# Performance work log

Hardware: AMD Instinct MI355X
Metric: run time of the kernel (lower is better)

## Reference

```python
import jax, jax.numpy as jnp
import numpy as np

SIGMA = 0.248
PRNUM = 6
P = 7.5
K = 3.0
ALPHA = 2.5


def _gauss_kernel():
    # 5x5 normalized Gaussian, replicated per channel for depthwise conv [O=3,I=1,5,5]
    x = jnp.arange(-2, 3, dtype=jnp.float32)
    x2, y2 = jnp.meshgrid(x, x, indexing='xy')
    k = jnp.exp(-(x2 ** 2 + y2 ** 2) / (2.0 * SIGMA ** 2))
    k = k / jnp.sum(k)
    return jnp.broadcast_to(k[None, None], (3, 1, 5, 5))


def _dwconv(x, k):
    # x: [3,H,W]; depthwise 5x5 conv, padding=2 (matches F.conv2d(..., padding=2, groups=3))
    return jax.lax.conv_general_dilated(
        x[None], k, window_strides=(1, 1), padding=[(2, 2), (2, 2)],
        feature_group_count=3, dimension_numbers=('NCHW', 'OIHW', 'NCHW'))[0]


def _down2(x):
    # torch bilinear align_corners=False at exact scale 0.5 == 2x2 average pooling
    c, h, w = x.shape
    return x.reshape(c, h // 2, 2, w // 2, 2).mean(axis=(2, 4))


def _up(x, hw):
    # torch bilinear align_corners=False upsample (half-pixel centers) == jax linear resize
    return jax.image.resize(x, (x.shape[0], hw[0], hw[1]), method='linear')


def _foveate(img, fixs):
    C, H, W = img.shape
    k = _gauss_kernel()
    # build Gaussian pyramid
    G = img
    pyr = [G]
    for _ in range(1, PRNUM):
        G = _down2(_dwconv(G, k))
        pyr.append(G)
    # re-expand each level back to full res (interpolate then blur at each step)
    As = [pyr[0]]
    for i in range(1, PRNUM):
        cur = pyr[i]
        for j in range(i):
            hw = (cur.shape[1] * 2, cur.shape[2] * 2) if j < i - 1 else (H, W)
            cur = _dwconv(_up(cur, hw), k)
        As.append(cur)
    As = jnp.stack(As)  # [prNum, 3, H, W]

    # radial eccentricity map (min distance over fixations)
    x = jnp.arange(W, dtype=jnp.float32)
    y = jnp.arange(H, dtype=jnp.float32)
    x2d, y2d = jnp.meshgrid(x, y, indexing='xy')  # each [H, W]
    d = jnp.sqrt((x2d[None] - fixs[:, 0, None, None]) ** 2 +
                 (y2d[None] - fixs[:, 1, None, None]) ** 2) / P
    theta = jnp.min(d, axis=0)
    R = ALPHA / (theta + ALPHA)

    Ts = [jnp.exp(-((2.0 ** (i - 3)) * R / SIGMA) ** 2 * K) for i in range(1, PRNUM)]
    Ts.append(jnp.zeros_like(R))

    om = np.minimum(np.sqrt(np.log(2.0) / K) / (2.0 ** np.arange(-2, 3)) * SIGMA, 1.0)
    omega = np.concatenate([om, [0.0]]).astype(np.float32)  # [prNum]

    layer_ind = jnp.zeros_like(R)
    for i in range(1, PRNUM):
        ind = (R >= omega[i]) & (R <= omega[i - 1])
        layer_ind = jnp.where(ind, jnp.float32(i), layer_ind)

    Bs = [(0.5 - Ts[i]) / (Ts[i - 1] - Ts[i] + 1e-5) for i in range(1, PRNUM)]

    Ms = []
    for i in range(PRNUM):
        base = jnp.ones_like(R) if i == 0 else 1.0 - Bs[i - 1]
        M = jnp.where(layer_ind == i, base, jnp.float32(0.0))
        if i < PRNUM - 1:
            M = jnp.where(layer_ind == i + 1, Bs[i], M)
        Ms.append(M)
    Ms = jnp.stack(Ms)  # [prNum, H, W]

    # blend: sum_p Ms[p] * As[p, c]
    im_fov = jnp.einsum('phw,pchw->chw', Ms, As)
    return im_fov


def setup_inputs() -> dict:
    key = jax.random.key(0)
    k1, k2 = jax.random.split(key)
    img = jax.random.uniform(k1, (3, 2048, 2048), dtype=jnp.float32) * 255.0
    fixs = jax.random.uniform(k2, (4, 2), dtype=jnp.float32) * 2048.0
    return {'img': img, 'fixs': fixs}


def reference(img, fixs):
    return _foveate(img, fixs)
```

## Files before the change

### kernel.cpp

```cpp
#include <hip/hip_runtime.h>
#include <math.h>

#define HW2048 (2048ull*2048ull)
typedef float f4 __attribute__((ext_vector_type(4)));
typedef float f2 __attribute__((ext_vector_type(2)));

struct BP {
  float P[4][3];
  float D2[5];
  float cc[5];
};

__device__ __forceinline__ int ladder5(float dd, const BP& bp) {
  return (dd >= bp.D2[0]) + (dd >= bp.D2[1]) + (dd >= bp.D2[2]) +
         (dd >= bp.D2[3]) + (dd >= bp.D2[4]);
}

__global__ __launch_bounds__(256) void downAll_k(const float* __restrict__ img,
                                                 float* __restrict__ C1,
                                                 float* __restrict__ p2,
                                                 float* __restrict__ p3,
                                                 float* __restrict__ p4,
                                                 float* __restrict__ p5,
                                                 const float* __restrict__ fixs,
                                                 int nf, float c1thr) {
  __shared__ float t2[16][17];
  __shared__ float t3[8][9];
  __shared__ float t4a[4][5];
  int tx = threadIdx.x, ty = threadIdx.y;
  int X = blockIdx.x * 16 + tx;
  int Y = blockIdx.y * 16 + ty;
  int c = blockIdx.z;

  int XB = blockIdx.x * 64, YB = blockIdx.y * 64;
  float bD = 3.4e38f;
  for (int f = 0; f < nf; ++f) {
    float fx = fixs[2 * f], fy = fixs[2 * f + 1];
    float dx = fmaxf(fmaxf((float)XB - fx, fx - (float)(XB + 63)), 0.f);
    float dy = fmaxf(fmaxf((float)YB - fy, fy - (float)(YB + 63)), 0.f);
    bD = fminf(bD, dx * dx + dy * dy);
  }
  bool wC1 = (bD <= c1thr);

  const float* ip = img + (size_t)c * HW2048 + (size_t)(4 * Y) * 2048 + 4 * X;
  f4 r0 = __builtin_nontemporal_load((const f4*)(ip));
  f4 r1 = __builtin_nontemporal_load((const f4*)(ip + 2048));
  f4 r2 = __builtin_nontemporal_load((const f4*)(ip + 4096));
  f4 r3 = __builtin_nontemporal_load((const f4*)(ip + 6144));
  float a00 = 0.25f * (r0.x + r0.y + r1.x + r1.y);
  float a01 = 0.25f * (r0.z + r0.w + r1.z + r1.w);
  float a10 = 0.25f * (r2.x + r2.y + r3.x + r3.y);
  float a11 = 0.25f * (r2.z + r2.w + r3.z + r3.w);
  if (wC1) {
    float* cp = C1 + (size_t)c * 1048576 + (size_t)(2 * Y) * 1024 + 2 * X;
    f2 u; u.x = a00; u.y = a01; *(f2*)cp = u;
    f2 v; v.x = a10; v.y = a11; *(f2*)(cp + 1024) = v;
  }
  float m = 0.25f * (a00 + a01 + a10 + a11);
  p2[((size_t)c * 512 + Y) * 512 + X] = m;
  t2[ty][tx] = m;
  __syncthreads();
  int tid = ty * 16 + tx;
  if (tid < 64) {
    int y = tid >> 3, x = tid & 7;
    float w = 0.25f * (t2[2*y][2*x] + t2[2*y][2*x+1] + t2[2*y+1][2*x] + t2[2*y+1][2*x+1]);
    p3[((size_t)c * 256 + blockIdx.y * 8 + y) * 256 + blockIdx.x * 8 + x] = w;
    t3[y][x] = w;
  }
  __syncthreads();
  if (tid < 16) {
    int y = tid >> 2, x = tid & 3;
    float w = 0.25f * (t3[2*y][2*x] + t3[2*y][2*x+1] + t3[2*y+1][2*x] + t3[2*y+1][2*x+1]);
    p4[((size_t)c * 128 + blockIdx.y * 4 + y) * 128 + blockIdx.x * 4 + x] = w;
    t4a[y][x] = w;
  }
  __syncthreads();
  if (tid < 4) {
    int y = tid >> 1, x = tid & 1;
    float w = 0.25f * (t4a[2*y][2*x] + t4a[2*y][2*x+1] + t4a[2*y+1][2*x] + t4a[2*y+1][2*x+1]);
    p5[((size_t)c * 64 + blockIdx.y * 2 + y) * 64 + blockIdx.x * 2 + x] = w;
  }
}

__device__ __forceinline__ void up_coords(int o, int n, int& i0, int& i1, float& w0) {
  int m = o >> 1;
  if (o & 1) { i0 = m; i1 = min(m + 1, n - 1); w0 = 0.75f; }
  else       { i0 = max(m - 1, 0); i1 = m;     w0 = 0.25f; }
}

__device__ __forceinline__ void s2c(const float* __restrict__ b, int x0, int y0,
                                    const BP& bp, float o[2][4]) {
  int t = x0 >> 2, ky = y0 >> 2, yph = y0 & 3;
  int c[3], r[3];
#pragma unroll
  for (int j = 0; j < 3; ++j) {
    c[j] = min(max(t - 1 + j, 0), 511);
    r[j] = min(max(ky - 1 + j, 0), 511);
  }
  float v[3][3];
#pragma unroll
  for (int j = 0; j < 3; ++j) {
    const float* row = b + r[j] * 512;
    v[j][0] = row[c[0]]; v[j][1] = row[c[1]]; v[j][2] = row[c[2]];
  }
  const float* wr0 = bp.P[yph];
  const float* wr1 = bp.P[yph + 1];
  float rv0[3], rv1[3];
#pragma unroll
  for (int i = 0; i < 3; ++i) {
    rv0[i] = wr0[0] * v[0][i] + wr0[1] * v[1][i] + wr0[2] * v[2][i];
    rv1[i] = wr1[0] * v[0][i] + wr1[1] * v[1][i] + wr1[2] * v[2][i];
  }
#pragma unroll
  for (int p = 0; p < 4; ++p) {
    o[0][p] = bp.P[p][0] * rv0[0] + bp.P[p][1] * rv0[1] + bp.P[p][2] * rv0[2];
    o[1][p] = bp.P[p][0] * rv1[0] + bp.P[p][1] * rv1[1] + bp.P[p][2] * rv1[2];
  }
}

__device__ __forceinline__ void s2c_lds(const float (*t)[68], int tx, int kyr, int yph,
                                        const BP& bp, float o[2][4]) {
  float v[3][3];
#pragma unroll
  for (int j = 0; j < 3; ++j) {
    const float* row = t[kyr + j];
    v[j][0] = row[tx]; v[j][1] = row[tx + 1]; v[j][2] = row[tx + 2];
  }
  const float* wr0 = bp.P[yph];
  const float* wr1 = bp.P[yph + 1];
  float rv0[3], rv1[3];
#pragma unroll
  for (int i = 0; i < 3; ++i) {
    rv0[i] = wr0[0] * v[0][i] + wr0[1] * v[1][i] + wr0[2] * v[2][i];
    rv1[i] = wr1[0] * v[0][i] + wr1[1] * v[1][i] + wr1[2] * v[2][i];
  }
#pragma unroll
  for (int p = 0; p < 4; ++p) {
    o[0][p] = bp.P[p][0] * rv0[0] + bp.P[p][1] * rv0[1] + bp.P[p][2] * rv0[2];
    o[1][p] = bp.P[p][0] * rv1[0] + bp.P[p][1] * rv1[1] + bp.P[p][2] * rv1[2];
  }
}

__device__ __forceinline__ void s1c(const float* __restrict__ b, int x0, int y0,
                                    float o[2][4]) {
  int q0 = x0 >> 1, qy = y0 >> 1;
  int c[4], r[3];
#pragma unroll
  for (int i = 0; i < 4; ++i) c[i] = min(max(q0 - 1 + i, 0), 1023);
#pragma unroll
  for (int j = 0; j < 3; ++j) r[j] = min(max(qy - 1 + j, 0), 1023);
  float v[3][4];
#pragma unroll
  for (int j = 0; j < 3; ++j) {
    const float* row = b + r[j] * 1024;
    v[j][0] = row[c[0]]; v[j][1] = row[c[1]]; v[j][2] = row[c[2]]; v[j][3] = row[c[3]];
  }
  float rv0[4], rv1[4];
#pragma unroll
  for (int i = 0; i < 4; ++i) {
    rv0[i] = 0.25f * v[0][i] + 0.75f * v[1][i];
    rv1[i] = 0.75f * v[1][i] + 0.25f * v[2][i];
  }
  o[0][0] = 0.25f * rv0[0] + 0.75f * rv0[1];
  o[0][1] = 0.75f * rv0[1] + 0.25f * rv0[2];
  o[0][2] = 0.25f * rv0[1] + 0.75f * rv0[2];
  o[0][3] = 0.75f * rv0[2] + 0.25f * rv0[3];
  o[1][0] = 0.25f * rv1[0] + 0.75f * rv1[1];
  o[1][1] = 0.75f * rv1[1] + 0.25f * rv1[2];
  o[1][2] = 0.25f * rv1[1] + 0.75f * rv1[2];
  o[1][3] = 0.75f * rv1[2] + 0.25f * rv1[3];
}

__device__ __forceinline__ void sampleL(
    int l, int ch, int x0, int y0, int tx, int kyr,
    const float* __restrict__ img, const float* __restrict__ C1,
    const float* __restrict__ p2,
    const float (*tU)[3][4][68], const BP& bp, float o[2][4]) {
  if (l == 0) {
    const float* imgc = img + (size_t)ch * HW2048;
    f4 v0 = *(const f4*)(imgc + (size_t)y0 * 2048 + x0);
    f4 v1 = *(const f4*)(imgc + (size_t)(y0 + 1) * 2048 + x0);
    o[0][0] = v0.x; o[0][1] = v0.y; o[0][2] = v0.z; o[0][3] = v0.w;
    o[1][0] = v1.x; o[1][1] = v1.y; o[1][2] = v1.z; o[1][3] = v1.w;
  } else if (l == 1) {
    s1c(C1 + (size_t)ch * 1048576, x0, y0, o);
  } else if (l == 2) {
    s2c(p2 + (size_t)ch * 262144, x0, y0, bp, o);
  } else {
    s2c_lds(tU[ch][l - 3], tx, kyr, y0 & 3, bp, o);
  }
}

__global__ __launch_bounds__(256) void fblend_k(
    const float* __restrict__ img, const float* __restrict__ C1,
    const float* __restrict__ p2, const float* __restrict__ p3,
    const float* __restrict__ p4, const float* __restrict__ p5,
    const float* __restrict__ fixs, int nf,
    float* __restrict__ out, BP bp) {
  __shared__ float tU[3][3][4][68];
  __shared__ float tM[3][2][5][38];
  __shared__ float tA[3][5][22];

  int tx = threadIdx.x, ty = threadIdx.y;
  int bx = blockIdx.x, by = blockIdx.y;
  int xs = bx * 64 + tx;
  int yp = by * 4 + ty;
  int x0 = xs * 4, y0 = yp * 2;
  size_t ob0 = (size_t)y0 * 2048 + x0;

  int X0 = bx * 256, Y0 = by * 8;
  float bDmin = 3.4e38f, bDmax = 3.4e38f;
  for (int f = 0; f < nf; ++f) {
    float fx = fixs[2 * f], fy = fixs[2 * f + 1];
    float dxm = fmaxf(fmaxf((float)X0 - fx, fx - (float)(X0 + 255)), 0.f);
    float dym = fmaxf(fmaxf((float)Y0 - fy, fy - (float)(Y0 + 7)), 0.f);
    bDmin = fminf(bDmin, dxm * dxm + dym * dym);
    float dxM = fmaxf(fx - (float)X0, (float)(X0 + 255) - fx);
    float dyM = fmaxf(fy - (float)Y0, (float)(Y0 + 7) - fy);
    bDmax = fminf(bDmax, dxM * dxM + dyM * dyM);
  }
  int bLmax = ladder5(bDmax + 2.0f, bp);
  int bLmin = ladder5(fmaxf(bDmin - 2.0f, 0.f), bp);

  if (bLmax == 0) {
#pragma unroll
    for (int ch = 0; ch < 3; ++ch) {
      const float* imgc = img + (size_t)ch * HW2048;
      f4 v0 = *(const f4*)(imgc + ob0);
      f4 v1 = *(const f4*)(imgc + ob0 + 2048);
      __builtin_nontemporal_store(v0, (f4*)(out + (size_t)ch * HW2048 + ob0));
      __builtin_nontemporal_store(v1, (f4*)(out + (size_t)ch * HW2048 + ob0 + 2048));
    }
    return;
  }

  int sLo = max(bLmin - 1, 3), sHi = min(bLmax, 5);
  int g0 = 2 * by - 1, c0 = 64 * bx - 1;
  if (sLo <= sHi) {
    int m0 = (g0 >> 1) - 1, n0 = (c0 >> 1) - 1;
    int q0 = (m0 >> 1) - 1, s0 = (n0 >> 1) - 1;
    bool lv5 = (sHi == 5), lv4 = (sLo <= 4 && sHi >= 4), lv3 = (sLo == 3);

    if (lv5 && tx < 20) {
#pragma unroll
      for (int rr = 0; rr < 2; ++rr) {
        int r = (rr == 0) ? ty : 4;
        if (rr == 0 || ty == 0) {
          int gy = min(max(q0 + r, 0), 127);
          int gx = min(max(s0 + tx, 0), 127);
          int r0, r1, e0, e1; float wy0, wx0;
          up_coords(gy, 64, r0, r1, wy0);
          up_coords(gx, 64, e0, e1, wx0);
          float wy1 = 1.f - wy0, wx1 = 1.f - wx0;
          int i00 = r0*64+e0, i01 = r0*64+e1, i10 = r1*64+e0, i11 = r1*64+e1;
#pragma unroll
          for (int ch = 0; ch < 3; ++ch) {
            const float* s = p5 + ch * 4096;
            tA[ch][r][tx] = wy0 * (wx0 * s[i00] + wx1 * s[i01])
                          + wy1 * (wx0 * s[i10] + wx1 * s[i11]);
          }
        }
      }
    }
    if (lv4 && tx < 36) {
#pragma unroll
      for (int rr = 0; rr < 2; ++rr) {
        int r = (rr == 0) ? ty : 4;
        if (rr == 0 || ty == 0) {
          int gy = min(max(m0 + r, 0), 255);
          int gx = min(max(n0 + tx, 0), 255);
          int r0, r1, e0, e1; float wy0, wx0;
          up_coords(gy, 128, r0, r1, wy0);
          up_coords(gx, 128, e0, e1, wx0);
          float wy1 = 1.f - wy0, wx1 = 1.f - wx0;
          int i00 = r0*128+e0, i01 = r0*128+e1, i10 = r1*128+e0, i11 = r1*128+e1;
#pragma unroll
          for (int ch = 0; ch < 3; ++ch) {
            const float* s = p4 + ch * 16384;
            tM[ch][0][r][tx] = wy0 * (wx0 * s[i00] + wx1 * s[i01])
                             + wy1 * (wx0 * s[i10] + wx1 * s[i11]);
          }
        }
      }
    }
    if (lv3) {
#pragma unroll
      for (int cc2 = 0; cc2 < 2; ++cc2) {
        int cI = (cc2 == 0) ? tx : 64 + tx;
        if (cc2 == 0 || tx < 2) {
          int gy = min(max(g0 + ty, 0), 511);
          int gx = min(max(c0 + cI, 0), 511);
          int r0, r1, e0, e1; float wy0, wx0;
          up_coords(gy, 256, r0, r1, wy0);
          up_coords(gx, 256, e0, e1, wx0);
          float wy1 = 1.f - wy0, wx1 = 1.f - wx0;
          int i00 = r0*256+e0, i01 = r0*256+e1, i10 = r1*256+e0, i11 = r1*256+e1;
#pragma unroll
          for (int ch = 0; ch < 3; ++ch) {
            const float* s = p3 + ch * 65536;
            tU[ch][0][ty][cI] = wy0 * (wx0 * s[i00] + wx1 * s[i01])
                              + wy1 * (wx0 * s[i10] + wx1 * s[i11]);
          }
        }
      }
    }
    __syncthreads();

    if (lv5 && tx < 36) {
#pragma unroll
      for (int rr = 0; rr < 2; ++rr) {
        int r = (rr == 0) ? ty : 4;
        if (rr == 0 || ty == 0) {
          int gy = min(max(m0 + r, 0), 255);
          int gx = min(max(n0 + tx, 0), 255);
          int r0, r1, e0, e1; float wy0, wx0;
          up_coords(gy, 128, r0, r1, wy0);
          up_coords(gx, 128, e0, e1, wx0);
          float wy1 = 1.f - wy0, wx1 = 1.f - wx0;
          int a0 = r0 - q0, a1 = r1 - q0, b0 = e0 - s0, b1 = e1 - s0;
#pragma unroll
          for (int ch = 0; ch < 3; ++ch)
            tM[ch][1][r][tx] = wy0 * (wx0 * tA[ch][a0][b0] + wx1 * tA[ch][a0][b1])
                             + wy1 * (wx0 * tA[ch][a1][b0] + wx1 * tA[ch][a1][b1]);
        }
      }
    }
    if (lv4) {
#pragma unroll
      for (int cc2 = 0; cc2 < 2; ++cc2) {
        int cI = (cc2 == 0) ? tx : 64 + tx;
        if (cc2 == 0 || tx < 2) {
          int gy = min(max(g0 + ty, 0), 511);
          int gx = min(max(c0 + cI, 0), 511);
          int r0, r1, e0, e1; float wy0, wx0;
          up_coords(gy, 256, r0, r1, wy0);
          up_coords(gx, 256, e0, e1, wx0);
          float wy1 = 1.f - wy0, wx1 = 1.f - wx0;
          int a0 = r0 - m0, a1 = r1 - m0, b0 = e0 - n0, b1 = e1 - n0;
#pragma unroll
          for (int ch = 0; ch < 3; ++ch)
            tU[ch][1][ty][cI] = wy0 * (wx0 * tM[ch][0][a0][b0] + wx1 * tM[ch][0][a0][b1])
                              + wy1 * (wx0 * tM[ch][0][a1][b0] + wx1 * tM[ch][0][a1][b1]);
        }
      }
    }
    __syncthreads();

    if (lv5) {
#pragma unroll
      for (int cc2 = 0; cc2 < 2; ++cc2) {
        int cI = (cc2 == 0) ? tx : 64 + tx;
        if (cc2 == 0 || tx < 2) {
          int gy = min(max(g0 + ty, 0), 511);
          int gx = min(max(c0 + cI, 0), 511);
          int r0, r1, e0, e1; float wy0, wx0;
          up_coords(gy, 256, r0, r1, wy0);
          up_coords(gx, 256, e0, e1, wx0);
          float wy1 = 1.f - wy0, wx1 = 1.f - wx0;
          int a0 = r0 - m0, a1 = r1 - m0, b0 = e0 - n0, b1 = e1 - n0;
#pragma unroll
          for (int ch = 0; ch < 3; ++ch)
            tU[ch][2][ty][cI] = wy0 * (wx0 * tM[ch][1][a0][b0] + wx1 * tM[ch][1][a0][b1])
                              + wy1 * (wx0 * tM[ch][1][a1][b0] + wx1 * tM[ch][1][a1][b1]);
        }
      }
    }
    __syncthreads();
  }

  float d2[2][4];
#pragma unroll
  for (int j = 0; j < 2; ++j)
#pragma unroll
    for (int i = 0; i < 4; ++i) d2[j][i] = 3.4e38f;
  for (int f = 0; f < nf; ++f) {
    float dx0 = (float)x0 - fixs[2 * f], dy0 = (float)y0 - fixs[2 * f + 1];
#pragma unroll
    for (int j = 0; j < 2; ++j) {
      float dy = dy0 + (float)j, dy2 = dy * dy;
#pragma unroll
      for (int i = 0; i < 4; ++i) {
        float dx = dx0 + (float)i;
        d2[j][i] = fminf(d2[j][i], dx * dx + dy2);
      }
    }
  }

  bool uniformB = (bLmin == bLmax);
  int lmax;
  bool mixed;
  if (uniformB) {
    lmax = bLmax; mixed = false;
  } else {
    float dmn = d2[0][0], dmx = d2[0][0];
#pragma unroll
    for (int j = 0; j < 2; ++j)
#pragma unroll
      for (int i = 0; i < 4; ++i) {
        dmn = fminf(dmn, d2[j][i]);
        dmx = fmaxf(dmx, d2[j][i]);
      }
    lmax = ladder5(dmx, bp);
    int lmin = ladder5(dmn, bp);
    mixed = (lmin != lmax);
  }

  if (lmax == 0) {
#pragma unroll
    for (int ch = 0; ch < 3; ++ch) {
      const float* imgc = img + (size_t)ch * HW2048;
      f4 v0 = *(const f4*)(imgc + ob0);
      f4 v1 = *(const f4*)(imgc + ob0 + 2048);
      __builtin_nontemporal_store(v0, (f4*)(out + (size_t)ch * HW2048 + ob0));
      __builtin_nontemporal_store(v1, (f4*)(out + (size_t)ch * HW2048 + ob0 + 2048));
    }
    return;
  }

  float thr  = (lmax == 1) ? bp.D2[0] : (lmax == 2) ? bp.D2[1] :
               (lmax == 3) ? bp.D2[2] : (lmax == 4) ? bp.D2[3] : bp.D2[4];
  float cm_A = (lmax == 1) ? bp.cc[0] : (lmax == 2) ? bp.cc[1] :
               (lmax == 3) ? bp.cc[2] : (lmax == 4) ? bp.cc[3] : bp.cc[4];
  float cm_B = (lmax <= 2) ? bp.cc[0] : (lmax == 3) ? bp.cc[1] :
               (lmax == 4) ? bp.cc[2] : bp.cc[3];
  bool top5 = (lmax >= 5);

  float Bv[2][4];
  bool  tp[2][4];
#pragma unroll
  for (int j = 0; j < 2; ++j)
#pragma unroll
    for (int i = 0; i < 4; ++i) {
      float dd = d2[j][i];
      bool top = uniformB ? true : (dd >= thr);
      tp[j][i] = top;
      float d = dd * __frsqrt_rn(dd);
      float R = 18.75f * __frcp_rn(d + 18.75f);
      float R2 = R * R;
      float cm = top ? cm_A : cm_B;
      float tsm = __expf(-cm * R2);
      float t2 = tsm * tsm;
      float tsL = (top && top5) ? 0.f : t2 * t2;
      float B = (0.5f - tsL) * __frcp_rn(tsm - tsL + 1e-5f);
      if (!top && lmax == 1) B = 0.f;
      Bv[j][i] = B;
    }

  int kyr = ty >> 1;
#pragma unroll
  for (int ch = 0; ch < 3; ++ch) {
    float sA[2][4], sB[2][4], sC[2][4];
    sampleL(lmax,     ch, x0, y0, tx, kyr, img, C1, p2, tU, bp, sA);
    sampleL(lmax - 1, ch, x0, y0, tx, kyr, img, C1, p2, tU, bp, sB);
#pragma unroll
    for (int j = 0; j < 2; ++j)
#pragma unroll
      for (int i = 0; i < 4; ++i) sC[j][i] = sB[j][i];
    if (mixed && lmax >= 2)
      sampleL(lmax - 2, ch, x0, y0, tx, kyr, img, C1, p2, tU, bp, sC);

    float res[2][4];
#pragma unroll
    for (int j = 0; j < 2; ++j)
#pragma unroll
      for (int i = 0; i < 4; ++i) {
        float B = Bv[j][i];
        bool top = tp[j][i];
        float hi = top ? sA[j][i] : sB[j][i];
        float lo = top ? sB[j][i] : sC[j][i];
        res[j][i] = B * lo + (1.f - B) * hi;
      }

    f4 v0, v1;
    v0.x = res[0][0]; v0.y = res[0][1]; v0.z = res[0][2]; v0.w = res[0][3];
    v1.x = res[1][0]; v1.y = res[1][1]; v1.z = res[1][2]; v1.w = res[1][3];
    __builtin_nontemporal_store(v0, (f4*)(out + (size_t)ch * HW2048 + ob0));
    __builtin_nontemporal_store(v1, (f4*)(out + (size_t)ch * HW2048 + ob0 + 2048));
  }
}

extern "C" void kernel_launch(void* const* d_in, const int* in_sizes, int n_in,
                              void* d_out, int out_size, void* d_ws, size_t ws_size,
                              hipStream_t stream) {
  const float* img  = (const float*)d_in[0];
  const float* fixs = (const float*)d_in[1];
  int nf = in_sizes[1] / 2;
  float* out = (float*)d_out;
  float* ws  = (float*)d_ws;

  BP bp;
  const double sig = 0.248, Kd = 3.0, Pd = 7.5, Ad = 2.5;
  double obv = sqrt(log(2.0) / Kd) * sig;
  for (int j = 0; j < 5; ++j) {
    double om = obv * pow(2.0, 2 - j);
    double Dj = Pd * Ad * (1.0 / om - 1.0);
    bp.D2[j] = (float)(Dj * Dj);
  }
  for (int X = 0; X < 5; ++X)
    bp.cc[X] = (float)(Kd * pow(2.0, 2.0 * (X - 2)) / (sig * sig));
  const float Pt[4][3] = {{0.375f, 0.625f, 0.f},
                          {0.1875f, 0.75f, 0.0625f},
                          {0.0625f, 0.75f, 0.1875f},
                          {0.f, 0.625f, 0.375f}};
  for (int a = 0; a < 4; ++a) for (int t = 0; t < 3; ++t) bp.P[a][t] = Pt[a][t];

  double rC1 = sqrt((double)bp.D2[3]) + 16.0;
  float c1thr = (float)(rC1 * rC1);

  size_t o = 0;
  float* C1 = ws + o; o += 3ull * 1024 * 1024;
  float* p2 = ws + o; o += 3ull * 512 * 512;
  float* p3 = ws + o; o += 3ull * 256 * 256;
  float* p4 = ws + o; o += 3ull * 128 * 128;
  float* p5 = ws + o; o += 3ull * 64 * 64;

  downAll_k <<<dim3(32, 32, 3), dim3(16, 16), 0, stream>>>(img, C1, p2, p3, p4, p5,
                                                           fixs, nf, c1thr);
  fblend_k  <<<dim3(8, 256),    dim3(64, 4),  0, stream>>>(img, C1, p2, p3, p4, p5,
                                                           fixs, nf, out, bp);
}
```

Measured before the change: 128.5 us.

## Gate p2 writes by eccentricity and fuse level-5 upsample chain into one stage

The downsample kernel now writes the p2 pyramid level only for tiles near a fixation, and the C1 write threshold is tightened to a lower level's radius. This cuts global write traffic. In the blend kernel, the level-5 two-step upsample no longer stages through a shared intermediate tile. Each thread composes both bilinear steps directly from the tA tile, which removes a barrier and a shared buffer but adds per-thread arithmetic. Correctness depends on the threshold radii covering every pixel whose blend weights reference C1 and p2.

```diff
diff --git a/kernel.cpp b/kernel.cpp
--- a/kernel.cpp
+++ b/kernel.cpp
@@ -23,7 +23,7 @@
                                                  float* __restrict__ p4,
                                                  float* __restrict__ p5,
                                                  const float* __restrict__ fixs,
-                                                 int nf, float c1thr) {
+                                                 int nf, float c1thr, float p2thr) {
   __shared__ float t2[16][17];
   __shared__ float t3[8][9];
   __shared__ float t4a[4][5];
@@ -41,6 +41,7 @@
     bD = fminf(bD, dx * dx + dy * dy);
   }
   bool wC1 = (bD <= c1thr);
+  bool wP2 = (bD <= p2thr);
 
   const float* ip = img + (size_t)c * HW2048 + (size_t)(4 * Y) * 2048 + 4 * X;
   f4 r0 = __builtin_nontemporal_load((const f4*)(ip));
@@ -57,7 +58,7 @@
     f2 v; v.x = a10; v.y = a11; *(f2*)(cp + 1024) = v;
   }
   float m = 0.25f * (a00 + a01 + a10 + a11);
-  p2[((size_t)c * 512 + Y) * 512 + X] = m;
+  if (wP2) p2[((size_t)c * 512 + Y) * 512 + X] = m;
   t2[ty][tx] = m;
   __syncthreads();
   int tid = ty * 16 + tx;
@@ -198,7 +199,7 @@
     const float* __restrict__ fixs, int nf,
     float* __restrict__ out, BP bp) {
   __shared__ float tU[3][3][4][68];
-  __shared__ float tM[3][2][5][38];
+  __shared__ float tM[3][5][38];
   __shared__ float tA[3][5][22];
 
   int tx = threadIdx.x, ty = threadIdx.y;
@@ -277,8 +278,8 @@
 #pragma unroll
           for (int ch = 0; ch < 3; ++ch) {
             const float* s = p4 + ch * 16384;
-            tM[ch][0][r][tx] = wy0 * (wx0 * s[i00] + wx1 * s[i01])
-                             + wy1 * (wx0 * s[i10] + wx1 * s[i11]);
+            tM[ch][r][tx] = wy0 * (wx0 * s[i00] + wx1 * s[i01])
+                          + wy1 * (wx0 * s[i10] + wx1 * s[i11]);
           }
         }
       }
@@ -306,62 +307,52 @@
     }
     __syncthreads();
 
-    if (lv5 && tx < 36) {
-#pragma unroll
-      for (int rr = 0; rr < 2; ++rr) {
-        int r = (rr == 0) ? ty : 4;
-        if (rr == 0 || ty == 0) {
-          int gy = min(max(m0 + r, 0), 255);
-          int gx = min(max(n0 + tx, 0), 255);
-          int r0, r1, e0, e1; float wy0, wx0;
-          up_coords(gy, 128, r0, r1, wy0);
-          up_coords(gx, 128, e0, e1, wx0);
-          float wy1 = 1.f - wy0, wx1 = 1.f - wx0;
-          int a0 = r0 - q0, a1 = r1 - q0, b0 = e0 - s0, b1 = e1 - s0;
-#pragma unroll
-          for (int ch = 0; ch < 3; ++ch)
-            tM[ch][1][r][tx] = wy0 * (wx0 * tA[ch][a0][b0] + wx1 * tA[ch][a0][b1])
-                             + wy1 * (wx0 * tA[ch][a1][b0] + wx1 * tA[ch][a1][b1]);
-        }
-      }
-    }
-    if (lv4) {
+    if (lv4 || lv5) {
 #pragma unroll
       for (int cc2 = 0; cc2 < 2; ++cc2) {
         int cI = (cc2 == 0) ? tx : 64 + tx;
         if (cc2 == 0 || tx < 2) {
           int gy = min(max(g0 + ty, 0), 511);
           int gx = min(max(c0 + cI, 0), 511);
-          int r0, r1, e0, e1; float wy0, wx0;
-          up_coords(gy, 256, r0, r1, wy0);
-          up_coords(gx, 256, e0, e1, wx0);
-          float wy1 = 1.f - wy0, wx1 = 1.f - wx0;
-          int a0 = r0 - m0, a1 = r1 - m0, b0 = e0 - n0, b1 = e1 - n0;
-#pragma unroll
-          for (int ch = 0; ch < 3; ++ch)
-            tU[ch][1][ty][cI] = wy0 * (wx0 * tM[ch][0][a0][b0] + wx1 * tM[ch][0][a0][b1])
-                              + wy1 * (wx0 * tM[ch][0][a1][b0] + wx1 * tM[ch][0][a1][b1]);
-        }
-      }
-    }
-    __syncthreads();
-
-    if (lv5) {
-#pragma unroll
-      for (int cc2 = 0; cc2 < 2; ++cc2) {
-        int cI = (cc2 == 0) ? tx : 64 + tx;
-        if (cc2 == 0 || tx < 2) {
-          int gy = min(max(g0 + ty, 0), 511);
-          int gx = min(max(c0 + cI, 0), 511);
-          int r0, r1, e0, e1; float wy0, wx0;
-          up_coords(gy, 256, r0, r1, wy0);
-          up_coords(gx, 256, e0, e1, wx0);
-          float wy1 = 1.f - wy0, wx1 = 1.f - wx0;
-          int a0 = r0 - m0, a1 = r1 - m0, b0 = e0 - n0, b1 = e1 - n0;
-#pragma unroll
-          for (int ch = 0; ch < 3; ++ch)
-            tU[ch][2][ty][cI] = wy0 * (wx0 * tM[ch][1][a0][b0] + wx1 * tM[ch][1][a0][b1])
-                              + wy1 * (wx0 * tM[ch][1][a1][b0] + wx1 * tM[ch][1][a1][b1]);
+          int R0, R1, E0, E1; float WY0, WX0;
+          up_coords(gy, 256, R0, R1, WY0);
+          up_coords(gx, 256, E0, E1, WX0);
+          float WY1 = 1.f - WY0, WX1 = 1.f - WX0;
+          if (lv4) {
+            int a0 = R0 - m0, a1 = R1 - m0, b0 = E0 - n0, b1 = E1 - n0;
+#pragma unroll
+            for (int ch = 0; ch < 3; ++ch)
+              tU[ch][1][ty][cI] = WY0 * (WX0 * tM[ch][a0][b0] + WX1 * tM[ch][a0][b1])
+                                + WY1 * (WX0 * tM[ch][a1][b0] + WX1 * tM[ch][a1][b1]);
+          }
+          if (lv5) {
+            int ra0[2], ra1[2]; float wv0[2];
+            up_coords(R0, 128, ra0[0], ra1[0], wv0[0]);
+            up_coords(R1, 128, ra0[1], ra1[1], wv0[1]);
+            int cb0[2], cb1[2]; float wu0[2];
+            up_coords(E0, 128, cb0[0], cb1[0], wu0[0]);
+            up_coords(E1, 128, cb0[1], cb1[1], wu0[1]);
+            int ia0[2] = {ra0[0] - q0, ra0[1] - q0};
+            int ia1[2] = {ra1[0] - q0, ra1[1] - q0};
+            int jb0[2] = {cb0[0] - s0, cb0[1] - s0};
+            int jb1[2] = {cb1[0] - s0, cb1[1] - s0};
+#pragma unroll
+            for (int ch = 0; ch < 3; ++ch) {
+              float tap[2][2];
+#pragma unroll
+              for (int a = 0; a < 2; ++a) {
+                float v0a = wv0[a], v1a = 1.f - wv0[a];
+#pragma unroll
+                for (int b = 0; b < 2; ++b) {
+                  float u0b = wu0[b], u1b = 1.f - wu0[b];
+                  tap[a][b] = v0a * (u0b * tA[ch][ia0[a]][jb0[b]] + u1b * tA[ch][ia0[a]][jb1[b]])
+                            + v1a * (u0b * tA[ch][ia1[a]][jb0[b]] + u1b * tA[ch][ia1[a]][jb1[b]]);
+                }
+              }
+              tU[ch][2][ty][cI] = WY0 * (WX0 * tap[0][0] + WX1 * tap[0][1])
+                                + WY1 * (WX0 * tap[1][0] + WX1 * tap[1][1]);
+            }
+          }
         }
       }
     }
@@ -504,8 +495,10 @@
                           {0.f, 0.625f, 0.375f}};
   for (int a = 0; a < 4; ++a) for (int t = 0; t < 3; ++t) bp.P[a][t] = Pt[a][t];
 
-  double rC1 = sqrt((double)bp.D2[3]) + 16.0;
+  double rC1 = sqrt((double)bp.D2[2]) + 16.0;
+  double rP2 = sqrt((double)bp.D2[3]) + 16.0;
   float c1thr = (float)(rC1 * rC1);
+  float p2thr = (float)(rP2 * rP2);
 
   size_t o = 0;
   float* C1 = ws + o; o += 3ull * 1024 * 1024;
@@ -515,7 +508,7 @@
   float* p5 = ws + o; o += 3ull * 64 * 64;
 
   downAll_k <<<dim3(32, 32, 3), dim3(16, 16), 0, stream>>>(img, C1, p2, p3, p4, p5,
-                                                           fixs, nf, c1thr);
+                                                           fixs, nf, c1thr, p2thr);
   fblend_k  <<<dim3(8, 256),    dim3(64, 4),  0, stream>>>(img, C1, p2, p3, p4, p5,
                                                            fixs, nf, out, bp);
 }
```

Result: no change. 127.3 us (median of 2 runs) (-0.9%).
